# Kernel tuning notes

Measured on AMD Instinct MI355X. Metric: run time of the kernel, lower is better.

The kernel has to match this reference:

```python
import jax, jax.numpy as jnp
import numpy as np

N, E = 50000, 800000
IN_CH, HID, OUT = 128, 64, 64
H1, H2 = 4, 1
NEG_SLOPE = 0.2  # PyG GATConv default


def _glorot(key, shape):
    fan_in, fan_out = shape[0], shape[-1]
    lim = (6.0 / (fan_in + fan_out)) ** 0.5
    return jax.random.uniform(key, shape, jnp.float32, -lim, lim)


def setup_inputs() -> dict:
    key = jax.random.key(0)
    ks = jax.random.split(key, 12)
    x = jax.random.normal(ks[0], (N, IN_CH), jnp.float32)
    edge_index = jax.random.randint(ks[1], (2, E), 0, N, jnp.int64)
    # layer 1: in_ch -> hid, 4 heads, concat
    W1 = _glorot(ks[2], (IN_CH, H1 * HID))
    a_src1 = _glorot(ks[3], (H1, HID))
    a_dst1 = _glorot(ks[4], (H1, HID))
    b1 = jnp.zeros((H1 * HID,), jnp.float32)
    # layer 2: hid*4 -> out, 1 head, mean (concat=False)
    W2 = _glorot(ks[5], (H1 * HID, H2 * OUT))
    a_src2 = _glorot(ks[6], (H2, OUT))
    a_dst2 = _glorot(ks[7], (H2, OUT))
    b2 = jnp.zeros((OUT,), jnp.float32)
    return {"x": x, "edge_index": edge_index, "W1": W1, "a_src1": a_src1,
            "a_dst1": a_dst1, "b1": b1, "W2": W2, "a_src2": a_src2,
            "a_dst2": a_dst2, "b2": b2}


def gat_layer(x, src, dst, W, a_src, a_dst, b, concat):
    n = x.shape[0]
    Hh, Fh = a_src.shape
    h = (x @ W).reshape(n, Hh, Fh)                      # [N,H,F]
    al_src = jnp.sum(h * a_src[None], axis=-1)          # [N,H]
    al_dst = jnp.sum(h * a_dst[None], axis=-1)          # [N,H]
    logits = jax.nn.leaky_relu(al_src[src] + al_dst[dst], NEG_SLOPE)  # [E,H]
    # numerically stable segment softmax over destination nodes
    mx = jax.ops.segment_max(logits, dst, num_segments=n)
    mx = jnp.where(jnp.isfinite(mx), mx, 0.0)
    e = jnp.exp(logits - mx[dst])                       # [E,H]
    denom = jax.ops.segment_sum(e, dst, num_segments=n)  # [N,H]
    alpha = e / jnp.maximum(denom[dst], 1e-16)          # [E,H]
    msg = h[src] * alpha[:, :, None]                    # [E,H,F]
    out = jax.ops.segment_sum(msg, dst, num_segments=n)  # [N,H,F]
    out = out.reshape(n, Hh * Fh) if concat else out.mean(axis=1)
    return out + b


def reference(x, edge_index, W1, a_src1, a_dst1, b1, W2, a_src2, a_dst2, b2):
    n = x.shape[0]
    # PyG GATConv adds self-loops by default
    loops = jnp.arange(n, dtype=edge_index.dtype)
    src = jnp.concatenate([edge_index[0], loops])
    dst = jnp.concatenate([edge_index[1], loops])
    h = gat_layer(x, src, dst, W1, a_src1, a_dst1, b1, concat=True)
    h = jax.nn.elu(h)
    # dropout is identity in eval mode
    out = gat_layer(h, src, dst, W2, a_src2, a_dst2, b2, concat=False)
    return out
```

## Files before the change

### kernel.cpp

```cpp
#include <hip/hip_runtime.h>
#include <math.h>

#define NEG_SLOPE 0.2f
#define SLOTS 64

typedef unsigned short ushort_t;
typedef _Float16 f16x8 __attribute__((ext_vector_type(8)));
typedef _Float16 h2v  __attribute__((ext_vector_type(2)));
typedef float f32x4v __attribute__((ext_vector_type(4)));

__device__ __forceinline__ float leaky(float x) { return x > 0.f ? x : NEG_SLOPE * x; }

__device__ __forceinline__ ushort_t f2h(float f) {
    union { _Float16 h; ushort_t u; } v; v.h = (_Float16)f; return v.u;
}
__device__ __forceinline__ float h2f(ushort_t u) {
    union { ushort_t u; _Float16 h; } v; v.u = u; return (float)v.h;
}
__device__ __forceinline__ unsigned packh(float a, float b) {
    union { h2v h; unsigned u; } c; c.h[0] = (_Float16)a; c.h[1] = (_Float16)b; return c.u;
}

__global__ __launch_bounds__(256) void k_prep1(const int* __restrict__ ei, int E, int EB,
                                               int* __restrict__ cnt, ushort_t* __restrict__ csr,
                                               const float* __restrict__ W1, const float* __restrict__ W2,
                                               const float* __restrict__ as1, const float* __restrict__ ad1,
                                               const float* __restrict__ as2, const float* __restrict__ ad2,
                                               ushort_t* __restrict__ W1t, ushort_t* __restrict__ W2t,
                                               float* __restrict__ va1s, float* __restrict__ va1d,
                                               float* __restrict__ va2s, float* __restrict__ va2d, int N) {
    int b = blockIdx.x;
    int t = threadIdx.x;
    if (b < EB) {
        int i = b * 256 + t;
        if (i < E) {
            int s = ei[i];
            int d = ei[E + i];
            int p = atomicAdd(&cnt[d], 1);
            if (p < SLOTS - 1) csr[d * SLOTS + 1 + p] = (ushort_t)s;
        }
        return;
    }
    b -= EB;
    if (b < 256) {
        if (t < 128) W1t[b * 128 + t] = f2h(W1[t * 256 + b]);
        return;
    } else if (b < 320) {
        int n = b - 256;
        W2t[n * 256 + t] = f2h(W2[t * 64 + n]);
        return;
    } else if (b == 320) {
        for (int idx = t; idx < 1024; idx += 256) {
            int k = idx >> 3, h = (idx >> 1) & 3, sd = idx & 1;
            const float* a = sd ? ad1 : as1;
            float acc = 0.f;
            for (int f = 0; f < 64; ++f) acc += W1[k * 256 + h * 64 + f] * a[h * 64 + f];
            (sd ? va1d : va1s)[k * 4 + h] = acc;
        }
        return;
    } else if (b == 321) {
        for (int idx = t; idx < 512; idx += 256) {
            int k = idx >> 1, sd = idx & 1;
            const float* a = sd ? ad2 : as2;
            float acc = 0.f;
            for (int f = 0; f < 64; ++f) acc += W2[k * 64 + f] * a[f];
            (sd ? va2d : va2s)[k] = acc;
        }
        return;
    }
    b -= 322;
    int n = b * 256 + t;
    if (n < N) csr[n * SLOTS] = (ushort_t)n;
}

__global__ __launch_bounds__(256) void k_gemm1(const float* __restrict__ x, const ushort_t* __restrict__ W1t,
                                               const float* __restrict__ va1s, const float* __restrict__ va1d,
                                               ushort_t* __restrict__ h1h,
                                               float4* __restrict__ alS, float4* __restrict__ alD, int N) {
    __shared__ ushort_t As[64 * 136];
    __shared__ ushort_t Bs[128 * 136];
    int t = threadIdx.x;
    int r0 = blockIdx.x * 64;
    int c0 = blockIdx.y * 128;
    #pragma unroll
    for (int q = 0; q < 4; ++q) {
        int idx = t + q * 256;
        int row = idx >> 4, off = idx & 15;
        int gr = r0 + row;
        uint4 pv = make_uint4(0, 0, 0, 0);
        if (gr < N) {
            const float* xp = x + (size_t)gr * 128 + off * 8;
            float4 f0 = *(const float4*)xp;
            float4 f1 = *(const float4*)(xp + 4);
            pv.x = packh(f0.x, f0.y); pv.y = packh(f0.z, f0.w);
            pv.z = packh(f1.x, f1.y); pv.w = packh(f1.z, f1.w);
        }
        *(uint4*)&As[row * 136 + off * 8] = pv;
    }
    #pragma unroll
    for (int q = 0; q < 8; ++q) {
        int idx = t + q * 256;
        int row = idx >> 4, off = idx & 15;
        uint4 v = *(const uint4*)(W1t + (size_t)(c0 + row) * 128 + off * 8);
        *(uint4*)&Bs[row * 136 + off * 8] = v;
    }
    __syncthreads();
    int w = t >> 6, lane = t & 63;
    int m = lane & 15, quad = lane >> 4;
    f32x4v acc[4][2];
    #pragma unroll
    for (int r = 0; r < 4; ++r)
        #pragma unroll
        for (int c = 0; c < 2; ++c)
            acc[r][c] = (f32x4v){0.f, 0.f, 0.f, 0.f};
    #pragma unroll
    for (int ks = 0; ks < 4; ++ks) {
        int k0 = ks * 32 + quad * 8;
        f16x8 af[4], bfr[2];
        #pragma unroll
        for (int r = 0; r < 4; ++r) af[r] = *(f16x8*)&As[(r * 16 + m) * 136 + k0];
        #pragma unroll
        for (int c = 0; c < 2; ++c) bfr[c] = *(f16x8*)&Bs[(w * 32 + c * 16 + m) * 136 + k0];
        #pragma unroll
        for (int r = 0; r < 4; ++r)
            #pragma unroll
            for (int c = 0; c < 2; ++c)
                acc[r][c] = __builtin_amdgcn_mfma_f32_16x16x32_f16(af[r], bfr[c], acc[r][c], 0, 0, 0);
    }
    #pragma unroll
    for (int r = 0; r < 4; ++r) {
        int gr0 = r0 + r * 16 + quad * 4;
        #pragma unroll
        for (int c = 0; c < 2; ++c) {
            int col = c0 + w * 32 + c * 16 + m;
            #pragma unroll
            for (int reg = 0; reg < 4; ++reg) {
                int gr = gr0 + reg;
                if (gr < N) h1h[(size_t)gr * 256 + col] = f2h(acc[r][c][reg]);
            }
        }
    }
    if (c0 == 0) {
        int r = t >> 2, kq = (t & 3) * 32;
        int gr = r0 + r;
        float s0 = 0, s1 = 0, s2 = 0, s3 = 0, d0 = 0, d1 = 0, d2 = 0, d3 = 0;
        for (int k = kq; k < kq + 32; ++k) {
            float xv = h2f(As[r * 136 + k]);
            float4 vs = *(const float4*)&va1s[k * 4];
            float4 vd = *(const float4*)&va1d[k * 4];
            s0 += xv * vs.x; s1 += xv * vs.y; s2 += xv * vs.z; s3 += xv * vs.w;
            d0 += xv * vd.x; d1 += xv * vd.y; d2 += xv * vd.z; d3 += xv * vd.w;
        }
        #pragma unroll
        for (int off = 1; off <= 2; off <<= 1) {
            s0 += __shfl_xor(s0, off, 64); s1 += __shfl_xor(s1, off, 64);
            s2 += __shfl_xor(s2, off, 64); s3 += __shfl_xor(s3, off, 64);
            d0 += __shfl_xor(d0, off, 64); d1 += __shfl_xor(d1, off, 64);
            d2 += __shfl_xor(d2, off, 64); d3 += __shfl_xor(d3, off, 64);
        }
        if ((t & 3) == 0 && gr < N) {
            alS[gr] = make_float4(s0, s1, s2, s3);
            alD[gr] = make_float4(d0, d1, d2, d3);
        }
    }
}

__global__ __launch_bounds__(256) void k_agg1(const int* __restrict__ cnt, const ushort_t* __restrict__ csr,
                                              const float4* __restrict__ alS4, const float4* __restrict__ alD4,
                                              const ushort_t* __restrict__ h1h, const float* __restrict__ b1,
                                              const float* __restrict__ va2s, const float* __restrict__ va2d,
                                              ushort_t* __restrict__ out1h,
                                              float* __restrict__ al2S, float* __restrict__ al2D, int N) {
    __shared__ float s_alpha[4][SLOTS + 1][4];
    __shared__ int   s_off[4][SLOTS + 1];
    int w = threadIdx.x >> 6, lane = threadIdx.x & 63;
    int n = blockIdx.x * 4 + w;
    if (n >= N) return;
    int stored = cnt[n]; if (stored > SLOTS - 1) stored = SLOTS - 1;
    int deg = stored + 1;
    float4 ald = alD4[n];

    float e0 = 0.f, e1 = 0.f, e2 = 0.f, e3 = 0.f;
    if (lane < deg) {
        int s = csr[n * SLOTS + lane];
        float4 as = alS4[s];
        e0 = __expf(leaky(as.x + ald.x));
        e1 = __expf(leaky(as.y + ald.y));
        e2 = __expf(leaky(as.z + ald.z));
        e3 = __expf(leaky(as.w + ald.w));
        s_off[w][lane] = s << 9;
        *(float4*)&s_alpha[w][lane][0] = make_float4(e0, e1, e2, e3);
    }
    if (lane == 0) {
        s_off[w][deg] = 0;
        *(float4*)&s_alpha[w][deg][0] = make_float4(0.f, 0.f, 0.f, 0.f);
    }
    float d0 = e0, d1 = e1, d2 = e2, d3 = e3;
    #pragma unroll
    for (int off = 32; off >= 1; off >>= 1) {
        d0 += __shfl_xor(d0, off, 64);
        d1 += __shfl_xor(d1, off, 64);
        d2 += __shfl_xor(d2, off, 64);
        d3 += __shfl_xor(d3, off, 64);
    }
    int half = lane >> 5, lid = lane & 31;
    int head = lid >> 3;
    float denh = head == 0 ? d0 : head == 1 ? d1 : head == 2 ? d2 : d3;
    float invh = 1.f / fmaxf(denh, 1e-16f);

    const char* hbase = (const char*)h1h;
    int choff = lid * 16;
    float facc[8] = {0.f, 0.f, 0.f, 0.f, 0.f, 0.f, 0.f, 0.f};
    int j0 = 0;
    for (; j0 + 8 <= deg; j0 += 8) {
        uint4 pbuf[4]; float abuf[4];
        #pragma unroll
        for (int i = 0; i < 4; ++i) {
            int jj = j0 + i * 2 + half;
            abuf[i] = s_alpha[w][jj][head];
            pbuf[i] = *(const uint4*)(hbase + s_off[w][jj] + choff);
        }
        h2v ha0 = (h2v)0, ha1 = (h2v)0, ha2 = (h2v)0, ha3 = (h2v)0;
        #pragma unroll
        for (int i = 0; i < 4; ++i) {
            union { uint4 u; h2v h[4]; } c; c.u = pbuf[i];
            _Float16 ah = (_Float16)abuf[i];
            h2v a2 = {ah, ah};
            ha0 += c.h[0] * a2; ha1 += c.h[1] * a2;
            ha2 += c.h[2] * a2; ha3 += c.h[3] * a2;
        }
        facc[0] += (float)ha0[0]; facc[1] += (float)ha0[1];
        facc[2] += (float)ha1[0]; facc[3] += (float)ha1[1];
        facc[4] += (float)ha2[0]; facc[5] += (float)ha2[1];
        facc[6] += (float)ha3[0]; facc[7] += (float)ha3[1];
    }
    if (j0 < deg) {
        h2v ha0 = (h2v)0, ha1 = (h2v)0, ha2 = (h2v)0, ha3 = (h2v)0;
        for (int j = j0; j < deg; j += 2) {
            int jj = j + half;
            float a = s_alpha[w][jj][head];
            union { uint4 u; h2v h[4]; } c;
            c.u = *(const uint4*)(hbase + s_off[w][jj] + choff);
            _Float16 ah = (_Float16)a;
            h2v a2 = {ah, ah};
            ha0 += c.h[0] * a2; ha1 += c.h[1] * a2;
            ha2 += c.h[2] * a2; ha3 += c.h[3] * a2;
        }
        facc[0] += (float)ha0[0]; facc[1] += (float)ha0[1];
        facc[2] += (float)ha1[0]; facc[3] += (float)ha1[1];
        facc[4] += (float)ha2[0]; facc[5] += (float)ha2[1];
        facc[6] += (float)ha3[0]; facc[7] += (float)ha3[1];
    }
    #pragma unroll
    for (int i = 0; i < 8; ++i) facc[i] += __shfl_xor(facc[i], 32, 64);

    int c8 = lid * 8;
    float4 bv0 = *(const float4*)&b1[c8];
    float4 bv1 = *(const float4*)&b1[c8 + 4];
    float v[8];
    v[0] = facc[0] * invh + bv0.x; v[1] = facc[1] * invh + bv0.y;
    v[2] = facc[2] * invh + bv0.z; v[3] = facc[3] * invh + bv0.w;
    v[4] = facc[4] * invh + bv1.x; v[5] = facc[5] * invh + bv1.y;
    v[6] = facc[6] * invh + bv1.z; v[7] = facc[7] * invh + bv1.w;
    #pragma unroll
    for (int i = 0; i < 8; ++i) v[i] = v[i] > 0.f ? v[i] : (__expf(v[i]) - 1.f);
    float4 vs0 = *(const float4*)&va2s[c8], vs1 = *(const float4*)&va2s[c8 + 4];
    float4 vd0 = *(const float4*)&va2d[c8], vd1 = *(const float4*)&va2d[c8 + 4];
    float ps = v[0]*vs0.x + v[1]*vs0.y + v[2]*vs0.z + v[3]*vs0.w
             + v[4]*vs1.x + v[5]*vs1.y + v[6]*vs1.z + v[7]*vs1.w;
    float pd = v[0]*vd0.x + v[1]*vd0.y + v[2]*vd0.z + v[3]*vd0.w
             + v[4]*vd1.x + v[5]*vd1.y + v[6]*vd1.z + v[7]*vd1.w;
    #pragma unroll
    for (int off = 16; off >= 1; off >>= 1) {
        ps += __shfl_xor(ps, off, 64);
        pd += __shfl_xor(pd, off, 64);
    }
    if (lane == 0) { al2S[n] = ps; al2D[n] = pd; }
    if (half == 0) {
        uint4 u;
        u.x = packh(v[0], v[1]); u.y = packh(v[2], v[3]);
        u.z = packh(v[4], v[5]); u.w = packh(v[6], v[7]);
        *(uint4*)(out1h + (size_t)n * 256 + c8) = u;
    }
}

__global__ __launch_bounds__(256) void k_gemm2(const ushort_t* __restrict__ in, const ushort_t* __restrict__ W2t,
                                               ushort_t* __restrict__ h2h, int N) {
    __shared__ ushort_t As[64 * 136];
    __shared__ ushort_t Bs[64 * 136];
    int t = threadIdx.x;
    int r0 = blockIdx.x * 64;
    int w = t >> 6, lane = t & 63;
    int m = lane & 15, quad = lane >> 4;
    f32x4v acc[4];
    #pragma unroll
    for (int r = 0; r < 4; ++r) acc[r] = (f32x4v){0.f, 0.f, 0.f, 0.f};
    for (int kb = 0; kb < 2; ++kb) {
        #pragma unroll
        for (int q = 0; q < 4; ++q) {
            int idx = t + q * 256;
            int row = idx >> 4, off = idx & 15;
            int gr = r0 + row;
            uint4 v = (gr < N) ? *(const uint4*)(in + (size_t)gr * 256 + kb * 128 + off * 8)
                               : make_uint4(0, 0, 0, 0);
            *(uint4*)&As[row * 136 + off * 8] = v;
        }
        #pragma unroll
        for (int q = 0; q < 4; ++q) {
            int idx = t + q * 256;
            int row = idx >> 4, off = idx & 15;
            uint4 v = *(const uint4*)(W2t + (size_t)row * 256 + kb * 128 + off * 8);
            *(uint4*)&Bs[row * 136 + off * 8] = v;
        }
        __syncthreads();
        #pragma unroll
        for (int ks = 0; ks < 4; ++ks) {
            int k0 = ks * 32 + quad * 8;
            f16x8 af[4], bfr;
            #pragma unroll
            for (int r = 0; r < 4; ++r) af[r] = *(f16x8*)&As[(r * 16 + m) * 136 + k0];
            bfr = *(f16x8*)&Bs[(w * 16 + m) * 136 + k0];
            #pragma unroll
            for (int r = 0; r < 4; ++r)
                acc[r] = __builtin_amdgcn_mfma_f32_16x16x32_f16(af[r], bfr, acc[r], 0, 0, 0);
        }
        __syncthreads();
    }
    int col = w * 16 + m;
    #pragma unroll
    for (int r = 0; r < 4; ++r) {
        int gr0 = r0 + r * 16 + quad * 4;
        #pragma unroll
        for (int reg = 0; reg < 4; ++reg) {
            int gr = gr0 + reg;
            if (gr < N) h2h[(size_t)gr * 64 + col] = f2h(acc[r][reg]);
        }
    }
}

__global__ __launch_bounds__(256) void k_agg2(const int* __restrict__ cnt, const ushort_t* __restrict__ csr,
                                              const float* __restrict__ alS, const float* __restrict__ alD,
                                              const ushort_t* __restrict__ h2h, const float* __restrict__ b2,
                                              float* __restrict__ out, int N) {
    int lane = threadIdx.x & 63;
    int n = blockIdx.x * 4 + (threadIdx.x >> 6);
    if (n >= N) return;
    int stored = cnt[n]; if (stored > SLOTS - 1) stored = SLOTS - 1;
    int deg = stored + 1;
    const ushort_t* crow = csr + (size_t)n * SLOTS;
    float ald = alD[n];

    int s0 = 0; float e0 = 0.f, den = 0.f;
    if (lane < deg) {
        s0 = crow[lane];
        e0 = __expf(leaky(alS[s0] + ald));
        den = e0;
    }
    #pragma unroll
    for (int off = 32; off >= 1; off >>= 1) den += __shfl_xor(den, off, 64);
    float inv = 1.f / fmaxf(den, 1e-16f);

    int grp = lane >> 3, cid = lane & 7;
    int choff = cid * 16;
    const char* hbase = (const char*)h2h;
    h2v ha0 = (h2v)0, ha1 = (h2v)0, ha2 = (h2v)0, ha3 = (h2v)0;
    for (int j = 0; j < deg; j += 8) {
        int jj = j + grp;
        float a = __shfl(e0, jj, 64);
        int s = __shfl(s0, jj, 64);
        union { uint4 u; h2v h[4]; } c;
        c.u = *(const uint4*)(hbase + ((size_t)s << 7) + choff);
        _Float16 ah = (_Float16)a;
        h2v a2 = {ah, ah};
        ha0 += c.h[0] * a2; ha1 += c.h[1] * a2;
        ha2 += c.h[2] * a2; ha3 += c.h[3] * a2;
    }
    float acc[8];
    acc[0] = (float)ha0[0]; acc[1] = (float)ha0[1];
    acc[2] = (float)ha1[0]; acc[3] = (float)ha1[1];
    acc[4] = (float)ha2[0]; acc[5] = (float)ha2[1];
    acc[6] = (float)ha3[0]; acc[7] = (float)ha3[1];
    #pragma unroll
    for (int off = 8; off <= 32; off <<= 1)
        #pragma unroll
        for (int i = 0; i < 8; ++i) acc[i] += __shfl_xor(acc[i], off, 64);

    if (grp == 0) {
        int c8 = cid * 8;
        float4 b0 = *(const float4*)&b2[c8];
        float4 b1v = *(const float4*)&b2[c8 + 4];
        float4 o0 = make_float4(acc[0]*inv + b0.x, acc[1]*inv + b0.y, acc[2]*inv + b0.z, acc[3]*inv + b0.w);
        float4 o1 = make_float4(acc[4]*inv + b1v.x, acc[5]*inv + b1v.y, acc[6]*inv + b1v.z, acc[7]*inv + b1v.w);
        *(float4*)(out + (size_t)n * 64 + c8) = o0;
        *(float4*)(out + (size_t)n * 64 + c8 + 4) = o1;
    }
}

extern "C" void kernel_launch(void* const* d_in, const int* in_sizes, int n_in,
                              void* d_out, int out_size, void* d_ws, size_t ws_size,
                              hipStream_t stream) {
    const float* x      = (const float*)d_in[0];
    const int*   ei     = (const int*)d_in[1];
    const float* W1     = (const float*)d_in[2];
    const float* a_src1 = (const float*)d_in[3];
    const float* a_dst1 = (const float*)d_in[4];
    const float* b1     = (const float*)d_in[5];
    const float* W2     = (const float*)d_in[6];
    const float* a_src2 = (const float*)d_in[7];
    const float* a_dst2 = (const float*)d_in[8];
    const float* b2     = (const float*)d_in[9];
    float* out = (float*)d_out;

    int N = in_sizes[0] / 128;
    int E = in_sizes[1] / 2;

    char* ws = (char*)d_ws;
    size_t off = 0;
    auto alloc = [&](size_t bytes) -> void* {
        void* p = ws + off;
        off = (off + bytes + 255) & ~(size_t)255;
        return p;
    };
    ushort_t* h1h   = (ushort_t*)alloc((size_t)N * 256 * 2);
    ushort_t* out1h = (ushort_t*)alloc((size_t)N * 256 * 2);
    ushort_t* h2h   = (ushort_t*)alloc((size_t)N * 64 * 2);
    ushort_t* W1t   = (ushort_t*)alloc(256 * 128 * 2);
    ushort_t* W2t   = (ushort_t*)alloc(64 * 256 * 2);
    float* va1s  = (float*)alloc(128 * 4 * 4);
    float* va1d  = (float*)alloc(128 * 4 * 4);
    float* va2s  = (float*)alloc(256 * 4);
    float* va2d  = (float*)alloc(256 * 4);
    float* alS1  = (float*)alloc((size_t)N * 4 * 4);
    float* alD1  = (float*)alloc((size_t)N * 4 * 4);
    float* alS2  = (float*)alloc((size_t)N * 4);
    float* alD2  = (float*)alloc((size_t)N * 4);
    int*   cnt   = (int*)alloc((size_t)N * 4);
    ushort_t* csr = (ushort_t*)alloc((size_t)N * SLOTS * 2);
    (void)ws_size; (void)n_in; (void)out_size;

    int EB  = (E + 255) / 256;
    int NB  = (N + 255) / 256;
    int GB1 = (N + 63) / 64;
    int NC4 = (N + 3) / 4;

    hipMemsetAsync(cnt, 0, (size_t)N * 4, stream);

    k_prep1<<<EB + 322 + NB, 256, 0, stream>>>(ei, E, EB, cnt, csr,
                                               W1, W2, a_src1, a_dst1, a_src2, a_dst2,
                                               W1t, W2t, va1s, va1d, va2s, va2d, N);
    dim3 g1(GB1, 2);
    k_gemm1<<<g1, 256, 0, stream>>>(x, W1t, va1s, va1d, h1h,
                                    (float4*)alS1, (float4*)alD1, N);
    k_agg1<<<NC4, 256, 0, stream>>>(cnt, csr,
                                    (const float4*)alS1, (const float4*)alD1,
                                    h1h, b1, va2s, va2d, out1h, alS2, alD2, N);
    k_gemm2<<<GB1, 256, 0, stream>>>(out1h, W2t, h2h, N);
    k_agg2<<<NC4, 256, 0, stream>>>(cnt, csr, alS2, alD2, h2h, b2, out, N);
}
```

Before: 268.9 us.

## Issue neighbor feature gathers before softmax in both aggregation kernels

```diff
diff --git a/kernel.cpp b/kernel.cpp
--- a/kernel.cpp
+++ b/kernel.cpp
@@ -165,36 +165,110 @@
     }
 }
 
+#define FLUSH_FACC() do { \
+    facc[0] += (float)ha0[0]; facc[1] += (float)ha0[1]; \
+    facc[2] += (float)ha1[0]; facc[3] += (float)ha1[1]; \
+    facc[4] += (float)ha2[0]; facc[5] += (float)ha2[1]; \
+    facc[6] += (float)ha3[0]; facc[7] += (float)ha3[1]; \
+    ha0 = (h2v)0; ha1 = (h2v)0; ha2 = (h2v)0; ha3 = (h2v)0; } while (0)
+
 __global__ __launch_bounds__(256) void k_agg1(const int* __restrict__ cnt, const ushort_t* __restrict__ csr,
                                               const float4* __restrict__ alS4, const float4* __restrict__ alD4,
                                               const ushort_t* __restrict__ h1h, const float* __restrict__ b1,
                                               const float* __restrict__ va2s, const float* __restrict__ va2d,
                                               ushort_t* __restrict__ out1h,
                                               float* __restrict__ al2S, float* __restrict__ al2D, int N) {
-    __shared__ float s_alpha[4][SLOTS + 1][4];
-    __shared__ int   s_off[4][SLOTS + 1];
+    __shared__ float s_alpha[4][SLOTS][4];
     int w = threadIdx.x >> 6, lane = threadIdx.x & 63;
     int n = blockIdx.x * 4 + w;
     if (n >= N) return;
     int stored = cnt[n]; if (stored > SLOTS - 1) stored = SLOTS - 1;
     int deg = stored + 1;
+
+    int s = 0;
+    if (lane < deg) s = csr[n * SLOTS + lane];
+
+    int half = lane >> 5, lid = lane & 31;
+    int head = lid >> 3;
+    int choff = lid * 16;
+    const char* hbase = (const char*)h1h;
+
+    uint4 pbuf[8];
+    #pragma unroll
+    for (int i = 0; i < 8; ++i) {
+        int sj = __shfl(s, i * 2 + half, 64);
+        pbuf[i] = *(const uint4*)(hbase + ((size_t)sj << 9) + choff);
+    }
+
     float4 ald = alD4[n];
-
     float e0 = 0.f, e1 = 0.f, e2 = 0.f, e3 = 0.f;
     if (lane < deg) {
-        int s = csr[n * SLOTS + lane];
         float4 as = alS4[s];
         e0 = __expf(leaky(as.x + ald.x));
         e1 = __expf(leaky(as.y + ald.y));
         e2 = __expf(leaky(as.z + ald.z));
         e3 = __expf(leaky(as.w + ald.w));
-        s_off[w][lane] = s << 9;
-        *(float4*)&s_alpha[w][lane][0] = make_float4(e0, e1, e2, e3);
-    }
-    if (lane == 0) {
-        s_off[w][deg] = 0;
-        *(float4*)&s_alpha[w][deg][0] = make_float4(0.f, 0.f, 0.f, 0.f);
-    }
+    }
+    *(float4*)&s_alpha[w][lane][0] = make_float4(e0, e1, e2, e3);
+
+    float facc[8] = {0.f, 0.f, 0.f, 0.f, 0.f, 0.f, 0.f, 0.f};
+    h2v ha0 = (h2v)0, ha1 = (h2v)0, ha2 = (h2v)0, ha3 = (h2v)0;
+    #pragma unroll
+    for (int i = 0; i < 4; ++i) {
+        float a = s_alpha[w][i * 2 + half][head];
+        union { uint4 u; h2v h[4]; } c; c.u = pbuf[i];
+        _Float16 ah = (_Float16)a;
+        h2v a2 = {ah, ah};
+        ha0 += c.h[0] * a2; ha1 += c.h[1] * a2;
+        ha2 += c.h[2] * a2; ha3 += c.h[3] * a2;
+    }
+    FLUSH_FACC();
+    #pragma unroll
+    for (int i = 4; i < 8; ++i) {
+        float a = s_alpha[w][i * 2 + half][head];
+        union { uint4 u; h2v h[4]; } c; c.u = pbuf[i];
+        _Float16 ah = (_Float16)a;
+        h2v a2 = {ah, ah};
+        ha0 += c.h[0] * a2; ha1 += c.h[1] * a2;
+        ha2 += c.h[2] * a2; ha3 += c.h[3] * a2;
+    }
+    FLUSH_FACC();
+
+    int j0 = 16;
+    for (; j0 + 8 <= deg; j0 += 8) {
+        uint4 pb[4]; float ab[4];
+        #pragma unroll
+        for (int i = 0; i < 4; ++i) {
+            int jj = j0 + i * 2 + half;
+            int sj = __shfl(s, jj, 64);
+            ab[i] = s_alpha[w][jj][head];
+            pb[i] = *(const uint4*)(hbase + ((size_t)sj << 9) + choff);
+        }
+        #pragma unroll
+        for (int i = 0; i < 4; ++i) {
+            union { uint4 u; h2v h[4]; } c; c.u = pb[i];
+            _Float16 ah = (_Float16)ab[i];
+            h2v a2 = {ah, ah};
+            ha0 += c.h[0] * a2; ha1 += c.h[1] * a2;
+            ha2 += c.h[2] * a2; ha3 += c.h[3] * a2;
+        }
+        FLUSH_FACC();
+    }
+    if (j0 < deg) {
+        for (int j = j0; j < deg; j += 2) {
+            int jj = j + half;
+            float a = s_alpha[w][jj][head];
+            int sj = __shfl(s, jj, 64);
+            union { uint4 u; h2v h[4]; } c;
+            c.u = *(const uint4*)(hbase + ((size_t)sj << 9) + choff);
+            _Float16 ah = (_Float16)a;
+            h2v a2 = {ah, ah};
+            ha0 += c.h[0] * a2; ha1 += c.h[1] * a2;
+            ha2 += c.h[2] * a2; ha3 += c.h[3] * a2;
+        }
+        FLUSH_FACC();
+    }
+
     float d0 = e0, d1 = e1, d2 = e2, d3 = e3;
     #pragma unroll
     for (int off = 32; off >= 1; off >>= 1) {
@@ -203,54 +277,9 @@
         d2 += __shfl_xor(d2, off, 64);
         d3 += __shfl_xor(d3, off, 64);
     }
-    int half = lane >> 5, lid = lane & 31;
-    int head = lid >> 3;
     float denh = head == 0 ? d0 : head == 1 ? d1 : head == 2 ? d2 : d3;
     float invh = 1.f / fmaxf(denh, 1e-16f);
 
-    const char* hbase = (const char*)h1h;
-    int choff = lid * 16;
-    float facc[8] = {0.f, 0.f, 0.f, 0.f, 0.f, 0.f, 0.f, 0.f};
-    int j0 = 0;
-    for (; j0 + 8 <= deg; j0 += 8) {
-        uint4 pbuf[4]; float abuf[4];
-        #pragma unroll
-        for (int i = 0; i < 4; ++i) {
-            int jj = j0 + i * 2 + half;
-            abuf[i] = s_alpha[w][jj][head];
-            pbuf[i] = *(const uint4*)(hbase + s_off[w][jj] + choff);
-        }
-        h2v ha0 = (h2v)0, ha1 = (h2v)0, ha2 = (h2v)0, ha3 = (h2v)0;
-        #pragma unroll
-        for (int i = 0; i < 4; ++i) {
-            union { uint4 u; h2v h[4]; } c; c.u = pbuf[i];
-            _Float16 ah = (_Float16)abuf[i];
-            h2v a2 = {ah, ah};
-            ha0 += c.h[0] * a2; ha1 += c.h[1] * a2;
-            ha2 += c.h[2] * a2; ha3 += c.h[3] * a2;
-        }
-        facc[0] += (float)ha0[0]; facc[1] += (float)ha0[1];
-        facc[2] += (float)ha1[0]; facc[3] += (float)ha1[1];
-        facc[4] += (float)ha2[0]; facc[5] += (float)ha2[1];
-        facc[6] += (float)ha3[0]; facc[7] += (float)ha3[1];
-    }
-    if (j0 < deg) {
-        h2v ha0 = (h2v)0, ha1 = (h2v)0, ha2 = (h2v)0, ha3 = (h2v)0;
-        for (int j = j0; j < deg; j += 2) {
-            int jj = j + half;
-            float a = s_alpha[w][jj][head];
-            union { uint4 u; h2v h[4]; } c;
-            c.u = *(const uint4*)(hbase + s_off[w][jj] + choff);
-            _Float16 ah = (_Float16)a;
-            h2v a2 = {ah, ah};
-            ha0 += c.h[0] * a2; ha1 += c.h[1] * a2;
-            ha2 += c.h[2] * a2; ha3 += c.h[3] * a2;
-        }
-        facc[0] += (float)ha0[0]; facc[1] += (float)ha0[1];
-        facc[2] += (float)ha1[0]; facc[3] += (float)ha1[1];
-        facc[4] += (float)ha2[0]; facc[5] += (float)ha2[1];
-        facc[6] += (float)ha3[0]; facc[7] += (float)ha3[1];
-    }
     #pragma unroll
     for (int i = 0; i < 8; ++i) facc[i] += __shfl_xor(facc[i], 32, 64);
 
@@ -283,6 +312,7 @@
         *(uint4*)(out1h + (size_t)n * 256 + c8) = u;
     }
 }
+#undef FLUSH_FACC
 
 __global__ __launch_bounds__(256) void k_gemm2(const ushort_t* __restrict__ in, const ushort_t* __restrict__ W2t,
                                                ushort_t* __restrict__ h2h, int N) {
@@ -348,33 +378,52 @@
     int stored = cnt[n]; if (stored > SLOTS - 1) stored = SLOTS - 1;
     int deg = stored + 1;
     const ushort_t* crow = csr + (size_t)n * SLOTS;
-    float ald = alD[n];
-
-    int s0 = 0; float e0 = 0.f, den = 0.f;
-    if (lane < deg) {
-        s0 = crow[lane];
-        e0 = __expf(leaky(alS[s0] + ald));
-        den = e0;
-    }
-    #pragma unroll
-    for (int off = 32; off >= 1; off >>= 1) den += __shfl_xor(den, off, 64);
-    float inv = 1.f / fmaxf(den, 1e-16f);
+
+    int s0 = 0;
+    if (lane < deg) s0 = crow[lane];
 
     int grp = lane >> 3, cid = lane & 7;
     int choff = cid * 16;
     const char* hbase = (const char*)h2h;
+
+    uint4 pbuf[3];
+    #pragma unroll
+    for (int i = 0; i < 3; ++i) {
+        int sj = __shfl(s0, i * 8 + grp, 64);
+        pbuf[i] = *(const uint4*)(hbase + ((size_t)sj << 7) + choff);
+    }
+
+    float ald = alD[n];
+    float e0 = 0.f;
+    if (lane < deg) e0 = __expf(leaky(alS[s0] + ald));
+
     h2v ha0 = (h2v)0, ha1 = (h2v)0, ha2 = (h2v)0, ha3 = (h2v)0;
-    for (int j = 0; j < deg; j += 8) {
-        int jj = j + grp;
-        float a = __shfl(e0, jj, 64);
-        int s = __shfl(s0, jj, 64);
-        union { uint4 u; h2v h[4]; } c;
-        c.u = *(const uint4*)(hbase + ((size_t)s << 7) + choff);
+    #pragma unroll
+    for (int i = 0; i < 3; ++i) {
+        float a = __shfl(e0, i * 8 + grp, 64);
+        union { uint4 u; h2v h[4]; } c; c.u = pbuf[i];
         _Float16 ah = (_Float16)a;
         h2v a2 = {ah, ah};
         ha0 += c.h[0] * a2; ha1 += c.h[1] * a2;
         ha2 += c.h[2] * a2; ha3 += c.h[3] * a2;
     }
+    for (int j = 24; j < deg; j += 8) {
+        int jj = j + grp;
+        float a = __shfl(e0, jj, 64);
+        int sj = __shfl(s0, jj, 64);
+        union { uint4 u; h2v h[4]; } c;
+        c.u = *(const uint4*)(hbase + ((size_t)sj << 7) + choff);
+        _Float16 ah = (_Float16)a;
+        h2v a2 = {ah, ah};
+        ha0 += c.h[0] * a2; ha1 += c.h[1] * a2;
+        ha2 += c.h[2] * a2; ha3 += c.h[3] * a2;
+    }
+
+    float den = e0;
+    #pragma unroll
+    for (int off = 32; off >= 1; off >>= 1) den += __shfl_xor(den, off, 64);
+    float inv = 1.f / fmaxf(den, 1e-16f);
+
     float acc[8];
     acc[0] = (float)ha0[0]; acc[1] = (float)ha0[1];
     acc[2] = (float)ha1[0]; acc[3] = (float)ha1[1];
```

New measurement: 271.1 us. No clear change (+0.8%).

## Aggregate raw fp16 features before the W1 projection, dropping the layer-1 GEMM kernel

Applied to the files above, without the earlier changes.

```diff
diff --git a/kernel.cpp b/kernel.cpp
--- a/kernel.cpp
+++ b/kernel.cpp
@@ -3,6 +3,7 @@
 
 #define NEG_SLOPE 0.2f
 #define SLOTS 64
+#define NPB 16
 
 typedef unsigned short ushort_t;
 typedef _Float16 f16x8 __attribute__((ext_vector_type(8)));
@@ -21,16 +22,45 @@
     union { h2v h; unsigned u; } c; c.h[0] = (_Float16)a; c.h[1] = (_Float16)b; return c.u;
 }
 
-__global__ __launch_bounds__(256) void k_prep1(const int* __restrict__ ei, int E, int EB,
-                                               int* __restrict__ cnt, ushort_t* __restrict__ csr,
-                                               const float* __restrict__ W1, const float* __restrict__ W2,
+__global__ __launch_bounds__(256) void k_prep0(const float* __restrict__ W1, const float* __restrict__ W2,
                                                const float* __restrict__ as1, const float* __restrict__ ad1,
                                                const float* __restrict__ as2, const float* __restrict__ ad2,
                                                ushort_t* __restrict__ W1t, ushort_t* __restrict__ W2t,
                                                float* __restrict__ va1s, float* __restrict__ va1d,
-                                               float* __restrict__ va2s, float* __restrict__ va2d, int N) {
-    int b = blockIdx.x;
-    int t = threadIdx.x;
+                                               float* __restrict__ va2s, float* __restrict__ va2d) {
+    int b = blockIdx.x, t = threadIdx.x;
+    if (b < 256) {
+        if (t < 128) W1t[b * 128 + t] = f2h(W1[t * 256 + b]);
+    } else if (b < 320) {
+        int n = b - 256;
+        W2t[n * 256 + t] = f2h(W2[t * 64 + n]);
+    } else if (b == 320) {
+        for (int idx = t; idx < 1024; idx += 256) {
+            int k = idx >> 3, h = (idx >> 1) & 3, sd = idx & 1;
+            const float* a = sd ? ad1 : as1;
+            float acc = 0.f;
+            for (int f = 0; f < 64; ++f) acc += W1[k * 256 + h * 64 + f] * a[h * 64 + f];
+            (sd ? va1d : va1s)[k * 4 + h] = acc;
+        }
+    } else {
+        for (int idx = t; idx < 512; idx += 256) {
+            int k = idx >> 1, sd = idx & 1;
+            const float* a = sd ? ad2 : as2;
+            float acc = 0.f;
+            for (int f = 0; f < 64; ++f) acc += W2[k * 64 + f] * a[f];
+            (sd ? va2d : va2s)[k] = acc;
+        }
+    }
+}
+
+__global__ __launch_bounds__(256) void k_prep1(const int* __restrict__ ei, int E, int EB,
+                                               int* __restrict__ cnt, ushort_t* __restrict__ csr,
+                                               const float* __restrict__ x,
+                                               const float* __restrict__ va1s, const float* __restrict__ va1d,
+                                               ushort_t* __restrict__ xh,
+                                               float4* __restrict__ alS, float4* __restrict__ alD,
+                                               int N, int NB) {
+    int b = blockIdx.x, t = threadIdx.x;
     if (b < EB) {
         int i = b * 256 + t;
         if (i < E) {
@@ -42,245 +72,192 @@
         return;
     }
     b -= EB;
-    if (b < 256) {
-        if (t < 128) W1t[b * 128 + t] = f2h(W1[t * 256 + b]);
+    if (b < NB) {
+        int n = b * 256 + t;
+        if (n < N) csr[n * SLOTS] = (ushort_t)n;
         return;
-    } else if (b < 320) {
-        int n = b - 256;
-        W2t[n * 256 + t] = f2h(W2[t * 64 + n]);
-        return;
-    } else if (b == 320) {
-        for (int idx = t; idx < 1024; idx += 256) {
-            int k = idx >> 3, h = (idx >> 1) & 3, sd = idx & 1;
-            const float* a = sd ? ad1 : as1;
-            float acc = 0.f;
-            for (int f = 0; f < 64; ++f) acc += W1[k * 256 + h * 64 + f] * a[h * 64 + f];
-            (sd ? va1d : va1s)[k * 4 + h] = acc;
-        }
-        return;
-    } else if (b == 321) {
-        for (int idx = t; idx < 512; idx += 256) {
-            int k = idx >> 1, sd = idx & 1;
-            const float* a = sd ? ad2 : as2;
-            float acc = 0.f;
-            for (int f = 0; f < 64; ++f) acc += W2[k * 64 + f] * a[f];
-            (sd ? va2d : va2s)[k] = acc;
-        }
-        return;
-    }
-    b -= 322;
-    int n = b * 256 + t;
-    if (n < N) csr[n * SLOTS] = (ushort_t)n;
-}
-
-__global__ __launch_bounds__(256) void k_gemm1(const float* __restrict__ x, const ushort_t* __restrict__ W1t,
-                                               const float* __restrict__ va1s, const float* __restrict__ va1d,
-                                               ushort_t* __restrict__ h1h,
-                                               float4* __restrict__ alS, float4* __restrict__ alD, int N) {
-    __shared__ ushort_t As[64 * 136];
-    __shared__ ushort_t Bs[128 * 136];
-    int t = threadIdx.x;
-    int r0 = blockIdx.x * 64;
-    int c0 = blockIdx.y * 128;
-    #pragma unroll
-    for (int q = 0; q < 4; ++q) {
-        int idx = t + q * 256;
-        int row = idx >> 4, off = idx & 15;
-        int gr = r0 + row;
-        uint4 pv = make_uint4(0, 0, 0, 0);
-        if (gr < N) {
-            const float* xp = x + (size_t)gr * 128 + off * 8;
-            float4 f0 = *(const float4*)xp;
-            float4 f1 = *(const float4*)(xp + 4);
-            pv.x = packh(f0.x, f0.y); pv.y = packh(f0.z, f0.w);
-            pv.z = packh(f1.x, f1.y); pv.w = packh(f1.z, f1.w);
-        }
-        *(uint4*)&As[row * 136 + off * 8] = pv;
-    }
-    #pragma unroll
-    for (int q = 0; q < 8; ++q) {
-        int idx = t + q * 256;
-        int row = idx >> 4, off = idx & 15;
-        uint4 v = *(const uint4*)(W1t + (size_t)(c0 + row) * 128 + off * 8);
-        *(uint4*)&Bs[row * 136 + off * 8] = v;
-    }
-    __syncthreads();
-    int w = t >> 6, lane = t & 63;
-    int m = lane & 15, quad = lane >> 4;
-    f32x4v acc[4][2];
-    #pragma unroll
-    for (int r = 0; r < 4; ++r)
-        #pragma unroll
-        for (int c = 0; c < 2; ++c)
-            acc[r][c] = (f32x4v){0.f, 0.f, 0.f, 0.f};
-    #pragma unroll
-    for (int ks = 0; ks < 4; ++ks) {
-        int k0 = ks * 32 + quad * 8;
-        f16x8 af[4], bfr[2];
-        #pragma unroll
-        for (int r = 0; r < 4; ++r) af[r] = *(f16x8*)&As[(r * 16 + m) * 136 + k0];
-        #pragma unroll
-        for (int c = 0; c < 2; ++c) bfr[c] = *(f16x8*)&Bs[(w * 32 + c * 16 + m) * 136 + k0];
-        #pragma unroll
-        for (int r = 0; r < 4; ++r)
-            #pragma unroll
-            for (int c = 0; c < 2; ++c)
-                acc[r][c] = __builtin_amdgcn_mfma_f32_16x16x32_f16(af[r], bfr[c], acc[r][c], 0, 0, 0);
-    }
-    #pragma unroll
-    for (int r = 0; r < 4; ++r) {
-        int gr0 = r0 + r * 16 + quad * 4;
-        #pragma unroll
-        for (int c = 0; c < 2; ++c) {
-            int col = c0 + w * 32 + c * 16 + m;
-            #pragma unroll
-            for (int reg = 0; reg < 4; ++reg) {
-                int gr = gr0 + reg;
-                if (gr < N) h1h[(size_t)gr * 256 + col] = f2h(acc[r][c][reg]);
-            }
-        }
-    }
-    if (c0 == 0) {
-        int r = t >> 2, kq = (t & 3) * 32;
-        int gr = r0 + r;
-        float s0 = 0, s1 = 0, s2 = 0, s3 = 0, d0 = 0, d1 = 0, d2 = 0, d3 = 0;
-        for (int k = kq; k < kq + 32; ++k) {
-            float xv = h2f(As[r * 136 + k]);
-            float4 vs = *(const float4*)&va1s[k * 4];
-            float4 vd = *(const float4*)&va1d[k * 4];
-            s0 += xv * vs.x; s1 += xv * vs.y; s2 += xv * vs.z; s3 += xv * vs.w;
-            d0 += xv * vd.x; d1 += xv * vd.y; d2 += xv * vd.z; d3 += xv * vd.w;
-        }
-        #pragma unroll
-        for (int off = 1; off <= 2; off <<= 1) {
-            s0 += __shfl_xor(s0, off, 64); s1 += __shfl_xor(s1, off, 64);
-            s2 += __shfl_xor(s2, off, 64); s3 += __shfl_xor(s3, off, 64);
-            d0 += __shfl_xor(d0, off, 64); d1 += __shfl_xor(d1, off, 64);
-            d2 += __shfl_xor(d2, off, 64); d3 += __shfl_xor(d3, off, 64);
-        }
-        if ((t & 3) == 0 && gr < N) {
-            alS[gr] = make_float4(s0, s1, s2, s3);
-            alD[gr] = make_float4(d0, d1, d2, d3);
-        }
+    }
+    b -= NB;
+    int r = b * 16 + (t >> 4);
+    int idx = t & 15;
+    if (r >= N) return;
+    const float* xr = x + (size_t)r * 128 + idx * 8;
+    float4 f0 = *(const float4*)xr;
+    float4 f1 = *(const float4*)(xr + 4);
+    uint4 pv;
+    pv.x = packh(f0.x, f0.y); pv.y = packh(f0.z, f0.w);
+    pv.z = packh(f1.x, f1.y); pv.w = packh(f1.z, f1.w);
+    *(uint4*)&xh[(size_t)r * 128 + idx * 8] = pv;
+    float xs[8] = {f0.x, f0.y, f0.z, f0.w, f1.x, f1.y, f1.z, f1.w};
+    float s0 = 0, s1 = 0, s2 = 0, s3 = 0, d0 = 0, d1 = 0, d2 = 0, d3 = 0;
+    #pragma unroll
+    for (int j = 0; j < 8; ++j) {
+        int k = idx * 8 + j;
+        float4 vs = *(const float4*)&va1s[k * 4];
+        float4 vd = *(const float4*)&va1d[k * 4];
+        s0 += xs[j] * vs.x; s1 += xs[j] * vs.y; s2 += xs[j] * vs.z; s3 += xs[j] * vs.w;
+        d0 += xs[j] * vd.x; d1 += xs[j] * vd.y; d2 += xs[j] * vd.z; d3 += xs[j] * vd.w;
+    }
+    #pragma unroll
+    for (int off = 8; off >= 1; off >>= 1) {
+        s0 += __shfl_xor(s0, off, 64); s1 += __shfl_xor(s1, off, 64);
+        s2 += __shfl_xor(s2, off, 64); s3 += __shfl_xor(s3, off, 64);
+        d0 += __shfl_xor(d0, off, 64); d1 += __shfl_xor(d1, off, 64);
+        d2 += __shfl_xor(d2, off, 64); d3 += __shfl_xor(d3, off, 64);
+    }
+    if (idx == 0) {
+        alS[r] = make_float4(s0, s1, s2, s3);
+        alD[r] = make_float4(d0, d1, d2, d3);
     }
 }
 
 __global__ __launch_bounds__(256) void k_agg1(const int* __restrict__ cnt, const ushort_t* __restrict__ csr,
                                               const float4* __restrict__ alS4, const float4* __restrict__ alD4,
-                                              const ushort_t* __restrict__ h1h, const float* __restrict__ b1,
+                                              const ushort_t* __restrict__ xh, const ushort_t* __restrict__ W1t,
+                                              const float* __restrict__ b1,
                                               const float* __restrict__ va2s, const float* __restrict__ va2d,
                                               ushort_t* __restrict__ out1h,
                                               float* __restrict__ al2S, float* __restrict__ al2D, int N) {
-    __shared__ float s_alpha[4][SLOTS + 1][4];
-    __shared__ int   s_off[4][SLOTS + 1];
-    int w = threadIdx.x >> 6, lane = threadIdx.x & 63;
-    int n = blockIdx.x * 4 + w;
-    if (n >= N) return;
-    int stored = cnt[n]; if (stored > SLOTS - 1) stored = SLOTS - 1;
-    int deg = stored + 1;
-    float4 ald = alD4[n];
-
-    float e0 = 0.f, e1 = 0.f, e2 = 0.f, e3 = 0.f;
-    if (lane < deg) {
-        int s = csr[n * SLOTS + lane];
-        float4 as = alS4[s];
-        e0 = __expf(leaky(as.x + ald.x));
-        e1 = __expf(leaky(as.y + ald.y));
-        e2 = __expf(leaky(as.z + ald.z));
-        e3 = __expf(leaky(as.w + ald.w));
-        s_off[w][lane] = s << 9;
-        *(float4*)&s_alpha[w][lane][0] = make_float4(e0, e1, e2, e3);
-    }
-    if (lane == 0) {
-        s_off[w][deg] = 0;
-        *(float4*)&s_alpha[w][deg][0] = make_float4(0.f, 0.f, 0.f, 0.f);
-    }
-    float d0 = e0, d1 = e1, d2 = e2, d3 = e3;
-    #pragma unroll
-    for (int off = 32; off >= 1; off >>= 1) {
-        d0 += __shfl_xor(d0, off, 64);
-        d1 += __shfl_xor(d1, off, 64);
-        d2 += __shfl_xor(d2, off, 64);
-        d3 += __shfl_xor(d3, off, 64);
-    }
-    int half = lane >> 5, lid = lane & 31;
-    int head = lid >> 3;
-    float denh = head == 0 ? d0 : head == 1 ? d1 : head == 2 ? d2 : d3;
-    float invh = 1.f / fmaxf(denh, 1e-16f);
-
-    const char* hbase = (const char*)h1h;
-    int choff = lid * 16;
-    float facc[8] = {0.f, 0.f, 0.f, 0.f, 0.f, 0.f, 0.f, 0.f};
-    int j0 = 0;
-    for (; j0 + 8 <= deg; j0 += 8) {
-        uint4 pbuf[4]; float abuf[4];
-        #pragma unroll
-        for (int i = 0; i < 4; ++i) {
-            int jj = j0 + i * 2 + half;
-            abuf[i] = s_alpha[w][jj][head];
-            pbuf[i] = *(const uint4*)(hbase + s_off[w][jj] + choff);
-        }
-        h2v ha0 = (h2v)0, ha1 = (h2v)0, ha2 = (h2v)0, ha3 = (h2v)0;
-        #pragma unroll
-        for (int i = 0; i < 4; ++i) {
-            union { uint4 u; h2v h[4]; } c; c.u = pbuf[i];
-            _Float16 ah = (_Float16)abuf[i];
-            h2v a2 = {ah, ah};
-            ha0 += c.h[0] * a2; ha1 += c.h[1] * a2;
-            ha2 += c.h[2] * a2; ha3 += c.h[3] * a2;
-        }
-        facc[0] += (float)ha0[0]; facc[1] += (float)ha0[1];
-        facc[2] += (float)ha1[0]; facc[3] += (float)ha1[1];
-        facc[4] += (float)ha2[0]; facc[5] += (float)ha2[1];
-        facc[6] += (float)ha3[0]; facc[7] += (float)ha3[1];
-    }
-    if (j0 < deg) {
-        h2v ha0 = (h2v)0, ha1 = (h2v)0, ha2 = (h2v)0, ha3 = (h2v)0;
-        for (int j = j0; j < deg; j += 2) {
-            int jj = j + half;
-            float a = s_alpha[w][jj][head];
-            union { uint4 u; h2v h[4]; } c;
-            c.u = *(const uint4*)(hbase + s_off[w][jj] + choff);
-            _Float16 ah = (_Float16)a;
-            h2v a2 = {ah, ah};
-            ha0 += c.h[0] * a2; ha1 += c.h[1] * a2;
-            ha2 += c.h[2] * a2; ha3 += c.h[3] * a2;
-        }
-        facc[0] += (float)ha0[0]; facc[1] += (float)ha0[1];
-        facc[2] += (float)ha1[0]; facc[3] += (float)ha1[1];
-        facc[4] += (float)ha2[0]; facc[5] += (float)ha2[1];
-        facc[6] += (float)ha3[0]; facc[7] += (float)ha3[1];
-    }
-    #pragma unroll
-    for (int i = 0; i < 8; ++i) facc[i] += __shfl_xor(facc[i], 32, 64);
-
-    int c8 = lid * 8;
-    float4 bv0 = *(const float4*)&b1[c8];
-    float4 bv1 = *(const float4*)&b1[c8 + 4];
-    float v[8];
-    v[0] = facc[0] * invh + bv0.x; v[1] = facc[1] * invh + bv0.y;
-    v[2] = facc[2] * invh + bv0.z; v[3] = facc[3] * invh + bv0.w;
-    v[4] = facc[4] * invh + bv1.x; v[5] = facc[5] * invh + bv1.y;
-    v[6] = facc[6] * invh + bv1.z; v[7] = facc[7] * invh + bv1.w;
-    #pragma unroll
-    for (int i = 0; i < 8; ++i) v[i] = v[i] > 0.f ? v[i] : (__expf(v[i]) - 1.f);
-    float4 vs0 = *(const float4*)&va2s[c8], vs1 = *(const float4*)&va2s[c8 + 4];
-    float4 vd0 = *(const float4*)&va2d[c8], vd1 = *(const float4*)&va2d[c8 + 4];
-    float ps = v[0]*vs0.x + v[1]*vs0.y + v[2]*vs0.z + v[3]*vs0.w
-             + v[4]*vs1.x + v[5]*vs1.y + v[6]*vs1.z + v[7]*vs1.w;
-    float pd = v[0]*vd0.x + v[1]*vd0.y + v[2]*vd0.z + v[3]*vd0.w
-             + v[4]*vd1.x + v[5]*vd1.y + v[6]*vd1.z + v[7]*vd1.w;
-    #pragma unroll
-    for (int off = 16; off >= 1; off >>= 1) {
-        ps += __shfl_xor(ps, off, 64);
-        pd += __shfl_xor(pd, off, 64);
-    }
-    if (lane == 0) { al2S[n] = ps; al2D[n] = pd; }
-    if (half == 0) {
-        uint4 u;
-        u.x = packh(v[0], v[1]); u.y = packh(v[2], v[3]);
-        u.z = packh(v[4], v[5]); u.w = packh(v[6], v[7]);
-        *(uint4*)(out1h + (size_t)n * 256 + c8) = u;
+    __shared__ ushort_t s_agg[NPB * 552];
+    __shared__ float s_inv[NPB][4];
+    __shared__ float s_al2[NPB][2];
+    int t = threadIdx.x;
+    int w = t >> 6, lane = t & 63;
+    int grp = lane >> 4, cid = lane & 15;
+    int nb = blockIdx.x * NPB;
+    if (t < NPB * 2) ((float*)s_al2)[t] = 0.f;
+
+    const char* xb = (const char*)xh;
+    for (int sub = 0; sub < 4; ++sub) {
+        int slot = w * 4 + sub;
+        int n = nb + slot;
+        int deg = 0, s = 0;
+        if (n < N) {
+            int stored = cnt[n]; if (stored > SLOTS - 1) stored = SLOTS - 1;
+            deg = stored + 1;
+            if (lane < deg) s = csr[(size_t)n * SLOTS + lane];
+        }
+        float e0 = 0.f, e1 = 0.f, e2 = 0.f, e3 = 0.f;
+        if (n < N && lane < deg) {
+            float4 ald = alD4[n];
+            float4 as = alS4[s];
+            e0 = __expf(leaky(as.x + ald.x));
+            e1 = __expf(leaky(as.y + ald.y));
+            e2 = __expf(leaky(as.z + ald.z));
+            e3 = __expf(leaky(as.w + ald.w));
+        }
+        float acc[32];
+        #pragma unroll
+        for (int i = 0; i < 32; ++i) acc[i] = 0.f;
+        int nit = (deg + 3) >> 2;
+        for (int j0 = 0; j0 < nit; j0 += 4) {
+            uint4 pb[4];
+            int nc = nit - j0; if (nc > 4) nc = 4;
+            #pragma unroll
+            for (int i = 0; i < 4; ++i) if (i < nc) {
+                int sj = __shfl(s, (j0 + i) * 4 + grp, 64);
+                pb[i] = *(const uint4*)(xb + ((size_t)sj << 8) + cid * 16);
+            }
+            #pragma unroll
+            for (int i = 0; i < 4; ++i) if (i < nc) {
+                int e = (j0 + i) * 4 + grp;
+                float a0 = __shfl(e0, e, 64), a1 = __shfl(e1, e, 64);
+                float a2 = __shfl(e2, e, 64), a3 = __shfl(e3, e, 64);
+                union { uint4 u; _Float16 f[8]; } cu; cu.u = pb[i];
+                #pragma unroll
+                for (int j = 0; j < 8; ++j) {
+                    float xv = (float)cu.f[j];
+                    acc[j]      += a0 * xv;
+                    acc[8 + j]  += a1 * xv;
+                    acc[16 + j] += a2 * xv;
+                    acc[24 + j] += a3 * xv;
+                }
+            }
+        }
+        #pragma unroll
+        for (int i = 0; i < 32; ++i) {
+            acc[i] += __shfl_xor(acc[i], 16, 64);
+            acc[i] += __shfl_xor(acc[i], 32, 64);
+        }
+        float d0 = e0, d1 = e1, d2 = e2, d3 = e3;
+        #pragma unroll
+        for (int off = 32; off >= 1; off >>= 1) {
+            d0 += __shfl_xor(d0, off, 64); d1 += __shfl_xor(d1, off, 64);
+            d2 += __shfl_xor(d2, off, 64); d3 += __shfl_xor(d3, off, 64);
+        }
+        if (lane == 0) {
+            s_inv[slot][0] = 1.f / fmaxf(d0, 1e-16f);
+            s_inv[slot][1] = 1.f / fmaxf(d1, 1e-16f);
+            s_inv[slot][2] = 1.f / fmaxf(d2, 1e-16f);
+            s_inv[slot][3] = 1.f / fmaxf(d3, 1e-16f);
+        }
+        if (grp == 0) {
+            #pragma unroll
+            for (int h = 0; h < 4; ++h) {
+                uint4 u;
+                u.x = packh(acc[h * 8 + 0], acc[h * 8 + 1]);
+                u.y = packh(acc[h * 8 + 2], acc[h * 8 + 3]);
+                u.z = packh(acc[h * 8 + 4], acc[h * 8 + 5]);
+                u.w = packh(acc[h * 8 + 6], acc[h * 8 + 7]);
+                *(uint4*)&s_agg[slot * 552 + h * 136 + cid * 8] = u;
+            }
+        }
+    }
+    __syncthreads();
+
+    int m = lane & 15, quad = lane >> 4;
+    f32x4v acc4[4];
+    #pragma unroll
+    for (int cg = 0; cg < 4; ++cg) acc4[cg] = (f32x4v){0.f, 0.f, 0.f, 0.f};
+    f16x8 af[4];
+    #pragma unroll
+    for (int ks = 0; ks < 4; ++ks)
+        af[ks] = *(f16x8*)&s_agg[m * 552 + w * 136 + ks * 32 + quad * 8];
+    #pragma unroll
+    for (int cg = 0; cg < 4; ++cg) {
+        #pragma unroll
+        for (int ks = 0; ks < 4; ++ks) {
+            f16x8 bf = *(f16x8*)&W1t[(size_t)(w * 64 + cg * 16 + m) * 128 + ks * 32 + quad * 8];
+            acc4[cg] = __builtin_amdgcn_mfma_f32_16x16x32_f16(af[ks], bf, acc4[cg], 0, 0, 0);
+        }
+    }
+    float ps[4] = {0, 0, 0, 0}, pd[4] = {0, 0, 0, 0};
+    #pragma unroll
+    for (int cg = 0; cg < 4; ++cg) {
+        int c = w * 64 + cg * 16 + m;
+        float bias = b1[c];
+        float v2s = va2s[c], v2d = va2d[c];
+        #pragma unroll
+        for (int reg = 0; reg < 4; ++reg) {
+            int slot = quad * 4 + reg;
+            int n = nb + slot;
+            float v = acc4[cg][reg] * s_inv[slot][w] + bias;
+            v = v > 0.f ? v : (__expf(v) - 1.f);
+            if (n < N) out1h[(size_t)n * 256 + c] = f2h(v);
+            ps[reg] += v * v2s;
+            pd[reg] += v * v2d;
+        }
+    }
+    #pragma unroll
+    for (int off = 1; off <= 8; off <<= 1) {
+        #pragma unroll
+        for (int reg = 0; reg < 4; ++reg) {
+            ps[reg] += __shfl_xor(ps[reg], off, 64);
+            pd[reg] += __shfl_xor(pd[reg], off, 64);
+        }
+    }
+    if (m == 0) {
+        #pragma unroll
+        for (int reg = 0; reg < 4; ++reg) {
+            int slot = quad * 4 + reg;
+            atomicAdd(&s_al2[slot][0], ps[reg]);
+            atomicAdd(&s_al2[slot][1], pd[reg]);
+        }
+    }
+    __syncthreads();
+    if (t < NPB) {
+        int n = nb + t;
+        if (n < N) { al2S[n] = s_al2[t][0]; al2D[n] = s_al2[t][1]; }
     }
 }
 
@@ -348,33 +325,52 @@
     int stored = cnt[n]; if (stored > SLOTS - 1) stored = SLOTS - 1;
     int deg = stored + 1;
     const ushort_t* crow = csr + (size_t)n * SLOTS;
-    float ald = alD[n];
-
-    int s0 = 0; float e0 = 0.f, den = 0.f;
-    if (lane < deg) {
-        s0 = crow[lane];
-        e0 = __expf(leaky(alS[s0] + ald));
-        den = e0;
-    }
-    #pragma unroll
-    for (int off = 32; off >= 1; off >>= 1) den += __shfl_xor(den, off, 64);
-    float inv = 1.f / fmaxf(den, 1e-16f);
+
+    int s0 = 0;
+    if (lane < deg) s0 = crow[lane];
 
     int grp = lane >> 3, cid = lane & 7;
     int choff = cid * 16;
     const char* hbase = (const char*)h2h;
+
+    uint4 pbuf[3];
+    #pragma unroll
+    for (int i = 0; i < 3; ++i) {
+        int sj = __shfl(s0, i * 8 + grp, 64);
+        pbuf[i] = *(const uint4*)(hbase + ((size_t)sj << 7) + choff);
+    }
+
+    float ald = alD[n];
+    float e0 = 0.f;
+    if (lane < deg) e0 = __expf(leaky(alS[s0] + ald));
+
     h2v ha0 = (h2v)0, ha1 = (h2v)0, ha2 = (h2v)0, ha3 = (h2v)0;
-    for (int j = 0; j < deg; j += 8) {
-        int jj = j + grp;
-        float a = __shfl(e0, jj, 64);
-        int s = __shfl(s0, jj, 64);
-        union { uint4 u; h2v h[4]; } c;
-        c.u = *(const uint4*)(hbase + ((size_t)s << 7) + choff);
+    #pragma unroll
+    for (int i = 0; i < 3; ++i) {
+        float a = __shfl(e0, i * 8 + grp, 64);
+        union { uint4 u; h2v h[4]; } c; c.u = pbuf[i];
         _Float16 ah = (_Float16)a;
         h2v a2 = {ah, ah};
         ha0 += c.h[0] * a2; ha1 += c.h[1] * a2;
         ha2 += c.h[2] * a2; ha3 += c.h[3] * a2;
     }
+    for (int j = 24; j < deg; j += 8) {
+        int jj = j + grp;
+        float a = __shfl(e0, jj, 64);
+        int sj = __shfl(s0, jj, 64);
+        union { uint4 u; h2v h[4]; } c;
+        c.u = *(const uint4*)(hbase + ((size_t)sj << 7) + choff);
+        _Float16 ah = (_Float16)a;
+        h2v a2 = {ah, ah};
+        ha0 += c.h[0] * a2; ha1 += c.h[1] * a2;
+        ha2 += c.h[2] * a2; ha3 += c.h[3] * a2;
+    }
+
+    float den = e0;
+    #pragma unroll
+    for (int off = 32; off >= 1; off >>= 1) den += __shfl_xor(den, off, 64);
+    float inv = 1.f / fmaxf(den, 1e-16f);
+
     float acc[8];
     acc[0] = (float)ha0[0]; acc[1] = (float)ha0[1];
     acc[2] = (float)ha1[0]; acc[3] = (float)ha1[1];
@@ -421,7 +417,7 @@
         off = (off + bytes + 255) & ~(size_t)255;
         return p;
     };
-    ushort_t* h1h   = (ushort_t*)alloc((size_t)N * 256 * 2);
+    ushort_t* xh    = (ushort_t*)alloc((size_t)N * 128 * 2);
     ushort_t* out1h = (ushort_t*)alloc((size_t)N * 256 * 2);
     ushort_t* h2h   = (ushort_t*)alloc((size_t)N * 64 * 2);
     ushort_t* W1t   = (ushort_t*)alloc(256 * 128 * 2);
@@ -440,20 +436,20 @@
 
     int EB  = (E + 255) / 256;
     int NB  = (N + 255) / 256;
+    int XB  = (N + 15) / 16;
     int GB1 = (N + 63) / 64;
+    int AB1 = (N + NPB - 1) / NPB;
     int NC4 = (N + 3) / 4;
 
     hipMemsetAsync(cnt, 0, (size_t)N * 4, stream);
 
-    k_prep1<<<EB + 322 + NB, 256, 0, stream>>>(ei, E, EB, cnt, csr,
-                                               W1, W2, a_src1, a_dst1, a_src2, a_dst2,
-                                               W1t, W2t, va1s, va1d, va2s, va2d, N);
-    dim3 g1(GB1, 2);
-    k_gemm1<<<g1, 256, 0, stream>>>(x, W1t, va1s, va1d, h1h,
-                                    (float4*)alS1, (float4*)alD1, N);
-    k_agg1<<<NC4, 256, 0, stream>>>(cnt, csr,
+    k_prep0<<<322, 256, 0, stream>>>(W1, W2, a_src1, a_dst1, a_src2, a_dst2,
+                                     W1t, W2t, va1s, va1d, va2s, va2d);
+    k_prep1<<<EB + NB + XB, 256, 0, stream>>>(ei, E, EB, cnt, csr, x, va1s, va1d,
+                                              xh, (float4*)alS1, (float4*)alD1, N, NB);
+    k_agg1<<<AB1, 256, 0, stream>>>(cnt, csr,
                                     (const float4*)alS1, (const float4*)alD1,
-                                    h1h, b1, va2s, va2d, out1h, alS2, alD2, N);
+                                    xh, W1t, b1, va2s, va2d, out1h, alS2, alD2, N);
     k_gemm2<<<GB1, 256, 0, stream>>>(out1h, W2t, h2h, N);
     k_agg2<<<NC4, 256, 0, stream>>>(cnt, csr, alS2, alD2, h2h, b2, out, N);
 }
```

Result: slower. 318.3 us (+18.4%).
